# Performance work log

Measured on AMD Instinct MI355X. Metric: run time of the kernel, lower is better.

Reference implementation:

```python
import jax, jax.numpy as jnp
import numpy as np

IN_F, OUT_F, BLOCK, NBLK = 1024, 4096, 256, 16
TOPK = NBLK // 4  # 4, as in forward: n_blocks // 4


def setup_inputs() -> dict:
    key = jax.random.key(0)
    ks = jax.random.split(key, 7)
    s = 1.0 / np.sqrt(IN_F)
    s2 = 1.0 / np.sqrt(OUT_F)
    return {
        "x": jax.random.normal(ks[0], (4, 4096, IN_F), jnp.float32),
        "router_w": jax.random.uniform(ks[1], (NBLK, IN_F), jnp.float32, -s, s),
        "router_b": jax.random.uniform(ks[2], (NBLK,), jnp.float32, -s, s),
        "w1": jax.random.uniform(ks[3], (OUT_F, IN_F), jnp.float32, -s, s),
        "b1": jax.random.uniform(ks[4], (OUT_F,), jnp.float32, -s, s),
        "w2": jax.random.uniform(ks[5], (IN_F, OUT_F), jnp.float32, -s2, s2),
        "b2": jax.random.uniform(ks[6], (IN_F,), jnp.float32, -s2, s2),
    }


def reference(x, router_w, router_b, w1, b1, w2, b2):
    x_shape = x.shape
    xf = x.reshape(-1, IN_F)  # [N, d]
    n = xf.shape[0]
    # router: Linear + softmax, then top-k block selection per token
    prob = jax.nn.softmax(xf @ router_w.T + router_b, axis=-1)  # [N, n_blocks]
    _, idx = jax.lax.top_k(prob, TOPK)  # [N, k]
    mask = jnp.zeros((n, NBLK), bool).at[jnp.arange(n)[:, None], idx].set(True)
    # RoutedLinearRow: per-block fc1, zeros at unselected blocks
    w1b = w1.reshape(NBLK, BLOCK, IN_F)
    b1b = b1.reshape(NBLK, BLOCK)
    h = jnp.einsum('nd,ibd->nib', xf, w1b) + b1b  # [N, n_blocks, block]
    h = jnp.where(mask[:, :, None], h, jnp.zeros((), h.dtype))
    h = jax.nn.relu(h)
    # RoutedLinearCol: only selected blocks contribute
    w2b = w2.reshape(IN_F, NBLK, BLOCK)
    y = jnp.einsum('nib,dib->nd', jnp.where(mask[:, :, None], h, 0.0), w2b) + b2
    return y.reshape(x_shape)
```

## Files before the change

kernel.cpp:

```cpp
#include <hip/hip_runtime.h>
#include <hip/hip_bf16.h>

#define NTOK   16384
#define INF    1024
#define OUTF   4096
#define NBLK   16
#define BLKSZ  256
#define KTOP   4

typedef short bf16x8 __attribute__((ext_vector_type(8)));
typedef float f32x4 __attribute__((ext_vector_type(4)));
typedef unsigned short u16x8 __attribute__((ext_vector_type(8)));

__device__ __forceinline__ unsigned short f2bf(float f) {
  unsigned u = __float_as_uint(f);
  u += 0x7FFFu + ((u >> 16) & 1u);
  return (unsigned short)(u >> 16);
}

__device__ __forceinline__ void load_lds16(const void* g, void* l) {
  __builtin_amdgcn_global_load_lds(
      (const __attribute__((address_space(1))) unsigned int*)g,
      (__attribute__((address_space(3))) unsigned int*)l, 16, 0, 0);
}

__device__ __forceinline__ double shfl_xor_d(double v, int m) {
  long long l = __double_as_longlong(v);
  int lo = (int)(l & 0xFFFFFFFFll), hi = (int)(l >> 32);
  lo = __shfl_xor(lo, m);
  hi = __shfl_xor(hi, m);
  return __longlong_as_double(((long long)hi << 32) | (unsigned long long)(unsigned)lo);
}

__device__ __forceinline__ int pi_perm(int j) {
  return (j & 128) | ((j & 7) << 4) | ((j >> 3) & 15);
}

__global__ __launch_bounds__(256) void k_convert(
    const float* __restrict__ w1, const float* __restrict__ w2,
    const float* __restrict__ b1, unsigned short* __restrict__ w1b,
    unsigned short* __restrict__ w2p, float* __restrict__ b1p,
    unsigned* __restrict__ counts) {
  if (blockIdx.x == 0 && threadIdx.x < 16) counts[threadIdx.x] = 0;
  const size_t stride = (size_t)gridDim.x * 256;
  for (size_t i = (size_t)blockIdx.x * 256 + threadIdx.x; i < 1573376; i += stride) {
    if (i < 1048576) {
      float4 v = ((const float4*)w1)[i];
      ushort4 o;
      o.x = f2bf(v.x); o.y = f2bf(v.y); o.z = f2bf(v.z); o.w = f2bf(v.w);
      ((ushort4*)w1b)[i] = o;
    } else if (i < 1572864) {
      const size_t g = i - 1048576;
      const int d = (int)(g >> 9);
      const int rest = (int)(g & 511);
      const int jg = rest * 8;
      const int blk = jg >> 8;
      const int j0 = jg & 255;
      const float* src = w2 + (size_t)d * 4096 + blk * 256;
      u16x8 o;
#pragma unroll
      for (int ni = 0; ni < 8; ++ni) o[ni] = f2bf(src[pi_perm(j0 + ni)]);
      *(u16x8*)(w2p + (size_t)d * 4096 + jg) = o;
    } else {
      const int idx = (int)(i - 1572864);
      const int jg = idx * 8;
      const int blk = jg >> 8;
      const int j0 = jg & 255;
      const float* src = b1 + blk * 256;
      float o[8];
#pragma unroll
      for (int ni = 0; ni < 8; ++ni) o[ni] = src[pi_perm(j0 + ni)];
      float4* dst = (float4*)(b1p + jg);
      dst[0] = make_float4(o[0], o[1], o[2], o[3]);
      dst[1] = make_float4(o[4], o[5], o[6], o[7]);
    }
  }
}

__global__ __launch_bounds__(256) void k_router(
    const float* __restrict__ x, const float* __restrict__ rw,
    const float* __restrict__ rb, unsigned* __restrict__ tok_blocks,
    unsigned* __restrict__ counts, unsigned short* __restrict__ xb) {
  __shared__ float4 rwl[4096];
  const int tid = threadIdx.x;
  const float4* rw4 = (const float4*)rw;
  for (int i = tid; i < 4096; i += 256) rwl[i] = rw4[i];
  __syncthreads();

  const int n = blockIdx.x * 32 + (tid >> 3);
  const int q = tid & 7;
  double p[16];
#pragma unroll
  for (int j = 0; j < 16; ++j) p[j] = 0.0;
  const float4* xr = (const float4*)(x + (size_t)n * INF);
  ushort4* xbr = (ushort4*)(xb + (size_t)n * INF);
#pragma unroll 4
  for (int i = 0; i < 32; ++i) {
    const int d4 = q + i * 8;
    const float4 xv = xr[d4];
    ushort4 o;
    o.x = f2bf(xv.x); o.y = f2bf(xv.y); o.z = f2bf(xv.z); o.w = f2bf(xv.w);
    xbr[d4] = o;
#pragma unroll
    for (int j = 0; j < 16; ++j) {
      const float4 wv = rwl[j * 256 + d4];
      p[j] = fma((double)xv.x, (double)wv.x, p[j]);
      p[j] = fma((double)xv.y, (double)wv.y, p[j]);
      p[j] = fma((double)xv.z, (double)wv.z, p[j]);
      p[j] = fma((double)xv.w, (double)wv.w, p[j]);
    }
  }
#pragma unroll
  for (int j = 0; j < 16; ++j) {
    double v = p[j];
    v += shfl_xor_d(v, 1);
    v += shfl_xor_d(v, 2);
    v += shfl_xor_d(v, 4);
    p[j] = v + (double)rb[j];
  }

  __syncthreads();
  unsigned* hist = (unsigned*)rwl;
  if (tid < 16) hist[tid] = 0;
  __syncthreads();

  if (q == 0) {
    unsigned packed = 0;
#pragma unroll
    for (int j = 0; j < 16; ++j) {
      int r = 0;
#pragma unroll
      for (int j2 = 0; j2 < 16; ++j2)
        r += (int)((p[j2] > p[j]) | ((p[j2] == p[j]) & (j2 < j)));
      if (r < KTOP) packed |= (unsigned)j << (8 * r);
    }
    tok_blocks[n] = packed;
    atomicAdd(&hist[packed & 15u], 1u);
    atomicAdd(&hist[(packed >> 8) & 15u], 1u);
    atomicAdd(&hist[(packed >> 16) & 15u], 1u);
    atomicAdd(&hist[(packed >> 24) & 15u], 1u);
  }
  __syncthreads();
  if (tid < 16 && hist[tid]) atomicAdd(&counts[tid], hist[tid]);
}

__global__ void k_scan(const unsigned* __restrict__ counts, unsigned* __restrict__ off,
                       unsigned* __restrict__ cursors) {
  if (threadIdx.x == 0 && blockIdx.x == 0) {
    unsigned o = 0;
    for (int i = 0; i < 16; ++i) {
      off[i] = o; cursors[i] = o;
      o += (counts[i] + 127u) & ~127u;
    }
    off[16] = o;
  }
}

__global__ __launch_bounds__(256) void k_build(
    const unsigned* __restrict__ tok_blocks, unsigned* __restrict__ cursors,
    unsigned short* __restrict__ list) {
  const int n = blockIdx.x * 256 + threadIdx.x;
  const unsigned packed = tok_blocks[n];
  const int lane = threadIdx.x & 63;
  for (int b = 0; b < 16; ++b) {
    int r = -1;
#pragma unroll
    for (int q = 0; q < 4; ++q)
      if (((packed >> (8 * q)) & 15u) == (unsigned)b) r = q;
    unsigned long long m = __ballot(r >= 0);
    if (m) {
      int leader = __ffsll((unsigned long long)m) - 1;
      unsigned base = 0;
      if (lane == leader) base = atomicAdd(&cursors[b], (unsigned)__popcll(m));
      base = (unsigned)__shfl((int)base, leader);
      if (r >= 0) {
        unsigned pos = base + (unsigned)__popcll(m & ((1ull << lane) - 1ull));
        list[pos] = (unsigned short)(n | (r << 14));
      }
    }
  }
}

__global__ __launch_bounds__(512, 1) void k_ffn(
    const unsigned short* __restrict__ xb, const unsigned short* __restrict__ w1b,
    const unsigned short* __restrict__ w2p, const float* __restrict__ b1p,
    const unsigned short* __restrict__ list, const unsigned* __restrict__ counts,
    const unsigned* __restrict__ off, unsigned short* __restrict__ part) {
  __shared__ __align__(16) char lds[163840];
  char* const As0 = lds + 65536;
  char* const As1 = lds + 81920;
  char* const Bs0 = lds + 98304;
  char* const Bs1 = lds + 131072;

  const int bid0 = blockIdx.x;
  const int bid = (bid0 & 7) * 256 + (bid0 >> 3);
  const int blk = bid >> 7;
  const int tile = bid & 127;
  const unsigned cnt = counts[blk];
  if ((unsigned)(tile * 128) >= cnt) return;
  const unsigned goff = off[blk] + tile * 128;
  const int rem = (int)cnt - tile * 128;

  const int tid = threadIdx.x;
  const int lane = tid & 63;
  const int wid = tid >> 6;
  const int wr = wid >> 1;
  const int wc = wid & 1;
  const int asl = tid & 7;
  const int c16 = lane & 15;

  const unsigned tok0 = list[goff + (tid >> 3)] & 0x3FFFu;
  const unsigned tok1 = list[goff + 64 + (tid >> 3)] & 0x3FFFu;
  const int arow0 = tid >> 3;
  const int arow1 = 64 + arow0;

  unsigned ep[2][4];
#pragma unroll
  for (int mi = 0; mi < 2; ++mi)
#pragma unroll
    for (int i = 0; i < 4; ++i)
      ep[mi][i] = list[goff + wr * 32 + mi * 16 + (lane >> 4) * 4 + i];

#define STAGE_A(buf, k0)                                                        \
  {                                                                             \
    load_lds16(xb + (size_t)tok0 * INF + (k0) + (asl ^ (arow0 & 7)) * 8,        \
               (buf) + (wid * 64) * 16);                                        \
    load_lds16(xb + (size_t)tok1 * INF + (k0) + (asl ^ (arow1 & 7)) * 8,        \
               (buf) + (512 + wid * 64) * 16);                                  \
  }

#define STAGE_B1(buf, k0)                                                       \
  _Pragma("unroll")                                                             \
  for (int r = 0; r < 4; ++r) {                                                 \
    const int row = (r * 512 + tid) >> 3;                                       \
    load_lds16(w1b + ((size_t)(blk * 256 + row)) * INF + (k0) +                 \
                   (asl ^ (row & 7)) * 8,                                       \
               (buf) + (r * 512 + wid * 64) * 16);                              \
  }

#define COMPUTE_A(abuf, bbuf)                                                   \
  _Pragma("unroll")                                                             \
  for (int ks = 0; ks < 2; ++ks) {                                              \
    const int kc = ks * 4 + (lane >> 4);                                        \
    bf16x8 a[2], b[8];                                                          \
    _Pragma("unroll")                                                           \
    for (int mi = 0; mi < 2; ++mi) {                                            \
      const int row = wr * 32 + mi * 16 + (lane & 15);                          \
      a[mi] = *(const bf16x8*)((abuf) + row * 128 + ((kc ^ (row & 7)) << 4));   \
    }                                                                           \
    _Pragma("unroll")                                                           \
    for (int ni = 0; ni < 8; ++ni) {                                            \
      const int row = wc * 128 + ni * 16 + (lane & 15);                         \
      b[ni] = *(const bf16x8*)((bbuf) + row * 128 + ((kc ^ (row & 7)) << 4));   \
    }                                                                           \
    _Pragma("unroll")                                                           \
    for (int mi = 0; mi < 2; ++mi)                                              \
      _Pragma("unroll")                                                         \
      for (int ni = 0; ni < 8; ++ni)                                            \
        acc[mi][ni] =                                                           \
            __builtin_amdgcn_mfma_f32_16x16x32_bf16(a[mi], b[ni], acc[mi][ni], 0, 0, 0); \
  }

  f32x4 acc[2][8] = {};
  STAGE_A(As0, 0);
  STAGE_B1(Bs0, 0);
  __syncthreads();
#pragma unroll 1
  for (int kk = 0; kk < 8; ++kk) {
    const int k0 = kk * 128;
    STAGE_A(As1, k0 + 64);
    STAGE_B1(Bs1, k0 + 64);
    COMPUTE_A(As0, Bs0);
    __syncthreads();
    if (kk < 7) {
      STAGE_A(As0, k0 + 128);
      STAGE_B1(Bs0, k0 + 128);
    }
    COMPUTE_A(As1, Bs1);
    __syncthreads();
  }

#define STAGE_B2(buf, it)                                                       \
  {                                                                             \
    const int ns2 = (it) >> 2, k02 = ((it) & 3) * 64;                           \
    _Pragma("unroll")                                                           \
    for (int r = 0; r < 4; ++r) {                                               \
      const int row = (r * 512 + tid) >> 3;                                     \
      load_lds16(w2p + (size_t)(ns2 * 256 + row) * OUTF + blk * 256 + k02 +     \
                     (asl ^ (row & 7)) * 8,                                     \
                 (buf) + (r * 512 + wid * 64) * 16);                            \
    }                                                                           \
  }

#define COMPUTE_B(bbuf, k02)                                                    \
  _Pragma("unroll")                                                             \
  for (int ks = 0; ks < 2; ++ks) {                                              \
    const int kc = ks * 4 + (lane >> 4);                                        \
    bf16x8 a[2], b[8];                                                          \
    _Pragma("unroll")                                                           \
    for (int mi = 0; mi < 2; ++mi) {                                            \
      const int row = wr * 32 + mi * 16 + (lane & 15);                          \
      a[mi] = *(const bf16x8*)(lds + row * 512 + (k02) * 2 +                    \
                               ((kc ^ (row & 7)) << 4));                        \
    }                                                                           \
    _Pragma("unroll")                                                           \
    for (int ni = 0; ni < 8; ++ni) {                                            \
      const int row = wc * 128 + ni * 16 + (lane & 15);                         \
      b[ni] = *(const bf16x8*)((bbuf) + row * 128 + ((kc ^ (row & 7)) << 4));   \
    }                                                                           \
    _Pragma("unroll")                                                           \
    for (int mi = 0; mi < 2; ++mi)                                              \
      _Pragma("unroll")                                                         \
      for (int ni = 0; ni < 8; ++ni)                                            \
        acc2[mi][ni] =                                                          \
            __builtin_amdgcn_mfma_f32_16x16x32_bf16(a[mi], b[ni], acc2[mi][ni], 0, 0, 0); \
  }

  STAGE_B2(Bs0, 0);

  {
    const float4* bp = (const float4*)(b1p + blk * 256 + wc * 128 + c16 * 8);
    const float4 bv0 = bp[0], bv1 = bp[1];
    const float bvv[8] = {bv0.x, bv0.y, bv0.z, bv0.w, bv1.x, bv1.y, bv1.z, bv1.w};
    const int chunk = wc * 16 + c16;
    const int cslot = (chunk & ~7);
    const int clow  = (chunk & 7);
#pragma unroll
    for (int mi = 0; mi < 2; ++mi) {
#pragma unroll
      for (int i = 0; i < 4; ++i) {
        const int row = wr * 32 + mi * 16 + (lane >> 4) * 4 + i;
        u16x8 wv;
#pragma unroll
        for (int ni = 0; ni < 8; ++ni) {
          float v = acc[mi][ni][i] + bvv[ni];
          v = v > 0.f ? v : 0.f;
          wv[ni] = f2bf(v);
        }
        *(u16x8*)(lds + row * 512 + ((cslot | (clow ^ (row & 7))) << 4)) = wv;
      }
    }
  }
  __syncthreads();

#pragma unroll 1
  for (int ns = 0; ns < 4; ++ns) {
    f32x4 acc2[2][8] = {};
    const int it0 = ns * 4;
    STAGE_B2(Bs1, it0 + 1);
    COMPUTE_B(Bs0, 0);
    __syncthreads();
    STAGE_B2(Bs0, it0 + 2);
    COMPUTE_B(Bs1, 64);
    __syncthreads();
    STAGE_B2(Bs1, it0 + 3);
    COMPUTE_B(Bs0, 128);
    __syncthreads();
    if (ns < 3) STAGE_B2(Bs0, it0 + 4);
    COMPUTE_B(Bs1, 192);
    __syncthreads();
#pragma unroll
    for (int mi = 0; mi < 2; ++mi) {
#pragma unroll
      for (int i = 0; i < 4; ++i) {
        const int row = wr * 32 + mi * 16 + (lane >> 4) * 4 + i;
        if (row < rem) {
          const unsigned e = ep[mi][i];
          u16x8 wv;
#pragma unroll
          for (int ni = 0; ni < 8; ++ni) wv[ni] = f2bf(acc2[mi][ni][i]);
          *(u16x8*)(part + ((size_t)(e & 0x3FFFu) * 4 + (e >> 14)) * 1024 +
                    ns * 256 + wc * 128 + c16 * 8) = wv;
        }
      }
    }
  }
#undef STAGE_A
#undef STAGE_B1
#undef STAGE_B2
#undef COMPUTE_A
#undef COMPUTE_B
}

__global__ __launch_bounds__(256) void k_reduce(const unsigned short* __restrict__ part,
                                                const float* __restrict__ b2,
                                                float* __restrict__ out) {
  __shared__ float lds[8 * 1028];
  const int tid = threadIdx.x;
  const int tok0 = blockIdx.x * 8;
  const int tok_l = tid >> 5;
  const int l32 = tid & 31;
  const unsigned short* pbase = part + (size_t)(tok0 + tok_l) * 4096;

#pragma unroll
  for (int g = 0; g < 4; ++g) {
    const int idx = g * 32 + l32;
    const int p0 = idx * 8;
    float s[8] = {0.f, 0.f, 0.f, 0.f, 0.f, 0.f, 0.f, 0.f};
#pragma unroll
    for (int sl = 0; sl < 4; ++sl) {
      u16x8 v = *(const u16x8*)(pbase + sl * 1024 + p0);
#pragma unroll
      for (int j = 0; j < 8; ++j)
        s[j] += __uint_as_float((unsigned)(unsigned short)v[j] << 16);
    }
    const int ns = idx >> 5, wcb = (idx >> 4) & 1, cc = idx & 15;
#pragma unroll
    for (int ni = 0; ni < 8; ++ni)
      lds[tok_l * 1028 + ns * 256 + wcb * 128 + ni * 16 + cc] = s[ni];
  }
  __syncthreads();
  const float4 b2v = ((const float4*)b2)[tid];
#pragma unroll
  for (int r = 0; r < 8; ++r) {
    f32x4 lv = *(f32x4*)&lds[r * 1028 + tid * 4];
    float4 o = make_float4(lv[0] + b2v.x, lv[1] + b2v.y, lv[2] + b2v.z, lv[3] + b2v.w);
    *(float4*)(out + (size_t)(tok0 + r) * 1024 + tid * 4) = o;
  }
}

extern "C" void kernel_launch(void* const* d_in, const int* in_sizes, int n_in,
                              void* d_out, int out_size, void* d_ws, size_t ws_size,
                              hipStream_t stream) {
  const float* x  = (const float*)d_in[0];
  const float* rw = (const float*)d_in[1];
  const float* rb = (const float*)d_in[2];
  const float* w1 = (const float*)d_in[3];
  const float* b1 = (const float*)d_in[4];
  const float* w2 = (const float*)d_in[5];
  const float* b2 = (const float*)d_in[6];
  float* out = (float*)d_out;

  char* ws = (char*)d_ws;
  unsigned short* part = (unsigned short*)(ws);
  unsigned short* xb   = (unsigned short*)(ws + 134217728);
  unsigned short* w1b  = (unsigned short*)(ws + 167772160);
  unsigned short* w2p  = (unsigned short*)(ws + 176160768);
  unsigned* tokb       = (unsigned*)(ws + 184549376);
  unsigned short* list = (unsigned short*)(ws + 184614912);
  float* b1p           = (float*)(ws + 184750080);
  unsigned* counts     = (unsigned*)(ws + 184766464);
  unsigned* off        = (unsigned*)(ws + 184766528);
  unsigned* cursors    = (unsigned*)(ws + 184766656);

  k_convert<<<dim3(1024), dim3(256), 0, stream>>>(w1, w2, b1, w1b, w2p, b1p, counts);
  k_router<<<dim3(512), dim3(256), 0, stream>>>(x, rw, rb, tokb, counts, xb);
  k_scan<<<dim3(1), dim3(64), 0, stream>>>(counts, off, cursors);
  k_build<<<dim3(64), dim3(256), 0, stream>>>(tokb, cursors, list);
  k_ffn<<<dim3(2048), dim3(512), 0, stream>>>(xb, w1b, w2p, b1p, list, counts, off, part);
  k_reduce<<<dim3(2048), dim3(256), 0, stream>>>(part, b2, out);
}
```

Measured before the change: 260.2 us.

## Fuse weight conversion into router, drop scan kernel, halve FFN block threads

Merges the weight-conversion kernel into the router kernel and removes the scan kernel. k_build and k_ffn now recompute the block offsets from counts, and counts/alloc are zeroed with a memset. The FFN kernel goes from 512 to 256 threads per block, so each wave handles 64 rows (4 MFMA row tiles) instead of 32. This doubles per-wave accumulator registers and A-fragment reuse. The goal is fewer launches and less LDS traffic per MFMA, at the risk of register pressure and lower wave count per CU.

```diff
diff --git a/kernel.cpp b/kernel.cpp
--- a/kernel.cpp
+++ b/kernel.cpp
@@ -36,14 +36,77 @@
   return (j & 128) | ((j & 7) << 4) | ((j >> 3) & 15);
 }
 
-__global__ __launch_bounds__(256) void k_convert(
-    const float* __restrict__ w1, const float* __restrict__ w2,
-    const float* __restrict__ b1, unsigned short* __restrict__ w1b,
-    unsigned short* __restrict__ w2p, float* __restrict__ b1p,
-    unsigned* __restrict__ counts) {
-  if (blockIdx.x == 0 && threadIdx.x < 16) counts[threadIdx.x] = 0;
+__global__ __launch_bounds__(256) void k_cvt_router(
+    const float* __restrict__ x, const float* __restrict__ rw,
+    const float* __restrict__ rb, const float* __restrict__ w1,
+    const float* __restrict__ w2, const float* __restrict__ b1,
+    unsigned* __restrict__ tok_blocks, unsigned* __restrict__ counts,
+    unsigned short* __restrict__ xb, unsigned short* __restrict__ w1b,
+    unsigned short* __restrict__ w2p, float* __restrict__ b1p) {
+  __shared__ float4 rwl[4096];
+  const int tid = threadIdx.x;
+  const float4* rw4 = (const float4*)rw;
+  for (int i = tid; i < 4096; i += 256) rwl[i] = rw4[i];
+  __syncthreads();
+
+  const int n = blockIdx.x * 32 + (tid >> 3);
+  const int q = tid & 7;
+  double p[16];
+#pragma unroll
+  for (int j = 0; j < 16; ++j) p[j] = 0.0;
+  const float4* xr = (const float4*)(x + (size_t)n * INF);
+  ushort4* xbr = (ushort4*)(xb + (size_t)n * INF);
+#pragma unroll 4
+  for (int i = 0; i < 32; ++i) {
+    const int d4 = q + i * 8;
+    const float4 xv = xr[d4];
+    ushort4 o;
+    o.x = f2bf(xv.x); o.y = f2bf(xv.y); o.z = f2bf(xv.z); o.w = f2bf(xv.w);
+    xbr[d4] = o;
+#pragma unroll
+    for (int j = 0; j < 16; ++j) {
+      const float4 wv = rwl[j * 256 + d4];
+      p[j] = fma((double)xv.x, (double)wv.x, p[j]);
+      p[j] = fma((double)xv.y, (double)wv.y, p[j]);
+      p[j] = fma((double)xv.z, (double)wv.z, p[j]);
+      p[j] = fma((double)xv.w, (double)wv.w, p[j]);
+    }
+  }
+#pragma unroll
+  for (int j = 0; j < 16; ++j) {
+    double v = p[j];
+    v += shfl_xor_d(v, 1);
+    v += shfl_xor_d(v, 2);
+    v += shfl_xor_d(v, 4);
+    p[j] = v + (double)rb[j];
+  }
+
+  __syncthreads();
+  unsigned* hist = (unsigned*)rwl;
+  if (tid < 16) hist[tid] = 0;
+  __syncthreads();
+
+  if (q == 0) {
+    unsigned packed = 0;
+#pragma unroll
+    for (int j = 0; j < 16; ++j) {
+      int r = 0;
+#pragma unroll
+      for (int j2 = 0; j2 < 16; ++j2)
+        r += (int)((p[j2] > p[j]) | ((p[j2] == p[j]) & (j2 < j)));
+      if (r < KTOP) packed |= (unsigned)j << (8 * r);
+    }
+    tok_blocks[n] = packed;
+    atomicAdd(&hist[packed & 15u], 1u);
+    atomicAdd(&hist[(packed >> 8) & 15u], 1u);
+    atomicAdd(&hist[(packed >> 16) & 15u], 1u);
+    atomicAdd(&hist[(packed >> 24) & 15u], 1u);
+  }
+  __syncthreads();
+  if (tid < 16 && hist[tid]) atomicAdd(&counts[tid], hist[tid]);
+
   const size_t stride = (size_t)gridDim.x * 256;
-  for (size_t i = (size_t)blockIdx.x * 256 + threadIdx.x; i < 1573376; i += stride) {
+  for (size_t i = (size_t)blockIdx.x * 256 + tid; i < 1573376; i += stride) {
     if (i < 1048576) {
       float4 v = ((const float4*)w1)[i];
       ushort4 o;
@@ -77,91 +140,19 @@
   }
 }
 
-__global__ __launch_bounds__(256) void k_router(
-    const float* __restrict__ x, const float* __restrict__ rw,
-    const float* __restrict__ rb, unsigned* __restrict__ tok_blocks,
-    unsigned* __restrict__ counts, unsigned short* __restrict__ xb) {
-  __shared__ float4 rwl[4096];
-  const int tid = threadIdx.x;
-  const float4* rw4 = (const float4*)rw;
-  for (int i = tid; i < 4096; i += 256) rwl[i] = rw4[i];
-  __syncthreads();
-
-  const int n = blockIdx.x * 32 + (tid >> 3);
-  const int q = tid & 7;
-  double p[16];
-#pragma unroll
-  for (int j = 0; j < 16; ++j) p[j] = 0.0;
-  const float4* xr = (const float4*)(x + (size_t)n * INF);
-  ushort4* xbr = (ushort4*)(xb + (size_t)n * INF);
-#pragma unroll 4
-  for (int i = 0; i < 32; ++i) {
-    const int d4 = q + i * 8;
-    const float4 xv = xr[d4];
-    ushort4 o;
-    o.x = f2bf(xv.x); o.y = f2bf(xv.y); o.z = f2bf(xv.z); o.w = f2bf(xv.w);
-    xbr[d4] = o;
-#pragma unroll
-    for (int j = 0; j < 16; ++j) {
-      const float4 wv = rwl[j * 256 + d4];
-      p[j] = fma((double)xv.x, (double)wv.x, p[j]);
-      p[j] = fma((double)xv.y, (double)wv.y, p[j]);
-      p[j] = fma((double)xv.z, (double)wv.z, p[j]);
-      p[j] = fma((double)xv.w, (double)wv.w, p[j]);
-    }
-  }
-#pragma unroll
-  for (int j = 0; j < 16; ++j) {
-    double v = p[j];
-    v += shfl_xor_d(v, 1);
-    v += shfl_xor_d(v, 2);
-    v += shfl_xor_d(v, 4);
-    p[j] = v + (double)rb[j];
-  }
-
-  __syncthreads();
-  unsigned* hist = (unsigned*)rwl;
-  if (tid < 16) hist[tid] = 0;
-  __syncthreads();
-
-  if (q == 0) {
-    unsigned packed = 0;
-#pragma unroll
-    for (int j = 0; j < 16; ++j) {
-      int r = 0;
-#pragma unroll
-      for (int j2 = 0; j2 < 16; ++j2)
-        r += (int)((p[j2] > p[j]) | ((p[j2] == p[j]) & (j2 < j)));
-      if (r < KTOP) packed |= (unsigned)j << (8 * r);
-    }
-    tok_blocks[n] = packed;
-    atomicAdd(&hist[packed & 15u], 1u);
-    atomicAdd(&hist[(packed >> 8) & 15u], 1u);
-    atomicAdd(&hist[(packed >> 16) & 15u], 1u);
-    atomicAdd(&hist[(packed >> 24) & 15u], 1u);
-  }
-  __syncthreads();
-  if (tid < 16 && hist[tid]) atomicAdd(&counts[tid], hist[tid]);
-}
-
-__global__ void k_scan(const unsigned* __restrict__ counts, unsigned* __restrict__ off,
-                       unsigned* __restrict__ cursors) {
-  if (threadIdx.x == 0 && blockIdx.x == 0) {
+__global__ __launch_bounds__(256) void k_build(
+    const unsigned* __restrict__ tok_blocks, const unsigned* __restrict__ counts,
+    unsigned* __restrict__ alloc, unsigned short* __restrict__ list) {
+  unsigned offl[16];
+  {
     unsigned o = 0;
-    for (int i = 0; i < 16; ++i) {
-      off[i] = o; cursors[i] = o;
-      o += (counts[i] + 127u) & ~127u;
-    }
-    off[16] = o;
-  }
-}
-
-__global__ __launch_bounds__(256) void k_build(
-    const unsigned* __restrict__ tok_blocks, unsigned* __restrict__ cursors,
-    unsigned short* __restrict__ list) {
+#pragma unroll
+    for (int i = 0; i < 16; ++i) { offl[i] = o; o += (counts[i] + 127u) & ~127u; }
+  }
   const int n = blockIdx.x * 256 + threadIdx.x;
   const unsigned packed = tok_blocks[n];
   const int lane = threadIdx.x & 63;
+#pragma unroll
   for (int b = 0; b < 16; ++b) {
     int r = -1;
 #pragma unroll
@@ -171,7 +162,7 @@
     if (m) {
       int leader = __ffsll((unsigned long long)m) - 1;
       unsigned base = 0;
-      if (lane == leader) base = atomicAdd(&cursors[b], (unsigned)__popcll(m));
+      if (lane == leader) base = offl[b] + atomicAdd(&alloc[b], (unsigned)__popcll(m));
       base = (unsigned)__shfl((int)base, leader);
       if (r >= 0) {
         unsigned pos = base + (unsigned)__popcll(m & ((1ull << lane) - 1ull));
@@ -181,11 +172,11 @@
   }
 }
 
-__global__ __launch_bounds__(512, 1) void k_ffn(
+__global__ __launch_bounds__(256, 1) void k_ffn(
     const unsigned short* __restrict__ xb, const unsigned short* __restrict__ w1b,
     const unsigned short* __restrict__ w2p, const float* __restrict__ b1p,
     const unsigned short* __restrict__ list, const unsigned* __restrict__ counts,
-    const unsigned* __restrict__ off, unsigned short* __restrict__ part) {
+    unsigned short* __restrict__ part) {
   __shared__ __align__(16) char lds[163840];
   char* const As0 = lds + 65536;
   char* const As1 = lds + 81920;
@@ -196,9 +187,18 @@
   const int bid = (bid0 & 7) * 256 + (bid0 >> 3);
   const int blk = bid >> 7;
   const int tile = bid & 127;
-  const unsigned cnt = counts[blk];
+  unsigned cnt = 0, goffBase = 0;
+  {
+    unsigned o = 0;
+#pragma unroll
+    for (int i = 0; i < 16; ++i) {
+      const unsigned c = counts[i];
+      if (i == blk) { cnt = c; goffBase = o; }
+      o += (c + 127u) & ~127u;
+    }
+  }
   if ((unsigned)(tile * 128) >= cnt) return;
-  const unsigned goff = off[blk] + tile * 128;
+  const unsigned goff = goffBase + tile * 128;
   const int rem = (int)cnt - tile * 128;
 
   const int tid = threadIdx.x;
@@ -206,62 +206,50 @@
   const int wid = tid >> 6;
   const int wr = wid >> 1;
   const int wc = wid & 1;
-  const int asl = tid & 7;
   const int c16 = lane & 15;
-
-  const unsigned tok0 = list[goff + (tid >> 3)] & 0x3FFFu;
-  const unsigned tok1 = list[goff + 64 + (tid >> 3)] & 0x3FFFu;
-  const int arow0 = tid >> 3;
-  const int arow1 = 64 + arow0;
-
-  unsigned ep[2][4];
-#pragma unroll
-  for (int mi = 0; mi < 2; ++mi)
-#pragma unroll
-    for (int i = 0; i < 4; ++i)
-      ep[mi][i] = list[goff + wr * 32 + mi * 16 + (lane >> 4) * 4 + i];
+  const int aChunk = (tid & 7) ^ ((tid >> 3) & 7);
+
+  unsigned tok[4];
+#pragma unroll
+  for (int l = 0; l < 4; ++l) tok[l] = list[goff + (tid >> 3) + l * 32] & 0x3FFFu;
 
 #define STAGE_A(buf, k0)                                                        \
-  {                                                                             \
-    load_lds16(xb + (size_t)tok0 * INF + (k0) + (asl ^ (arow0 & 7)) * 8,        \
-               (buf) + (wid * 64) * 16);                                        \
-    load_lds16(xb + (size_t)tok1 * INF + (k0) + (asl ^ (arow1 & 7)) * 8,        \
-               (buf) + (512 + wid * 64) * 16);                                  \
-  }
+  _Pragma("unroll")                                                             \
+  for (int l = 0; l < 4; ++l)                                                   \
+    load_lds16(xb + (size_t)tok[l] * 1024 + (k0) + aChunk * 8,                  \
+               (buf) + (l * 256 + wid * 64) * 16);
 
 #define STAGE_B1(buf, k0)                                                       \
   _Pragma("unroll")                                                             \
-  for (int r = 0; r < 4; ++r) {                                                 \
-    const int row = (r * 512 + tid) >> 3;                                       \
-    load_lds16(w1b + ((size_t)(blk * 256 + row)) * INF + (k0) +                 \
-                   (asl ^ (row & 7)) * 8,                                       \
-               (buf) + (r * 512 + wid * 64) * 16);                              \
-  }
+  for (int l = 0; l < 8; ++l)                                                   \
+    load_lds16(w1b + (size_t)(blk * 256 + l * 32 + (tid >> 3)) * 1024 + (k0) +  \
+                   aChunk * 8,                                                  \
+               (buf) + (l * 256 + wid * 64) * 16);
 
 #define COMPUTE_A(abuf, bbuf)                                                   \
   _Pragma("unroll")                                                             \
   for (int ks = 0; ks < 2; ++ks) {                                              \
     const int kc = ks * 4 + (lane >> 4);                                        \
-    bf16x8 a[2], b[8];                                                          \
-    _Pragma("unroll")                                                           \
-    for (int mi = 0; mi < 2; ++mi) {                                            \
-      const int row = wr * 32 + mi * 16 + (lane & 15);                          \
+    bf16x8 a[4], b[8];                                                          \
+    _Pragma("unroll")                                                           \
+    for (int mi = 0; mi < 4; ++mi) {                                            \
+      const int row = wr * 64 + mi * 16 + c16;                                  \
       a[mi] = *(const bf16x8*)((abuf) + row * 128 + ((kc ^ (row & 7)) << 4));   \
     }                                                                           \
     _Pragma("unroll")                                                           \
     for (int ni = 0; ni < 8; ++ni) {                                            \
-      const int row = wc * 128 + ni * 16 + (lane & 15);                         \
+      const int row = wc * 128 + ni * 16 + c16;                                 \
       b[ni] = *(const bf16x8*)((bbuf) + row * 128 + ((kc ^ (row & 7)) << 4));   \
     }                                                                           \
     _Pragma("unroll")                                                           \
-    for (int mi = 0; mi < 2; ++mi)                                              \
+    for (int mi = 0; mi < 4; ++mi)                                              \
       _Pragma("unroll")                                                         \
       for (int ni = 0; ni < 8; ++ni)                                            \
         acc[mi][ni] =                                                           \
             __builtin_amdgcn_mfma_f32_16x16x32_bf16(a[mi], b[ni], acc[mi][ni], 0, 0, 0); \
   }
 
-  f32x4 acc[2][8] = {};
+  f32x4 acc[4][8] = {};
   STAGE_A(As0, 0);
   STAGE_B1(Bs0, 0);
   __syncthreads();
@@ -284,32 +272,30 @@
   {                                                                             \
     const int ns2 = (it) >> 2, k02 = ((it) & 3) * 64;                           \
     _Pragma("unroll")                                                           \
-    for (int r = 0; r < 4; ++r) {                                               \
-      const int row = (r * 512 + tid) >> 3;                                     \
-      load_lds16(w2p + (size_t)(ns2 * 256 + row) * OUTF + blk * 256 + k02 +     \
-                     (asl ^ (row & 7)) * 8,                                     \
-                 (buf) + (r * 512 + wid * 64) * 16);                            \
-    }                                                                           \
+    for (int l = 0; l < 8; ++l)                                                 \
+      load_lds16(w2p + (size_t)(ns2 * 256 + l * 32 + (tid >> 3)) * 4096 +       \
+                     blk * 256 + k02 + aChunk * 8,                              \
+                 (buf) + (l * 256 + wid * 64) * 16);                            \
   }
 
 #define COMPUTE_B(bbuf, k02)                                                    \
   _Pragma("unroll")                                                             \
   for (int ks = 0; ks < 2; ++ks) {                                              \
     const int kc = ks * 4 + (lane >> 4);                                        \
-    bf16x8 a[2], b[8];                                                          \
-    _Pragma("unroll")                                                           \
-    for (int mi = 0; mi < 2; ++mi) {                                            \
-      const int row = wr * 32 + mi * 16 + (lane & 15);                          \
+    bf16x8 a[4], b[8];                                                          \
+    _Pragma("unroll")                                                           \
+    for (int mi = 0; mi < 4; ++mi) {                                            \
+      const int row = wr * 64 + mi * 16 + c16;                                  \
       a[mi] = *(const bf16x8*)(lds + row * 512 + (k02) * 2 +                    \
                                ((kc ^ (row & 7)) << 4));                        \
     }                                                                           \
     _Pragma("unroll")                                                           \
     for (int ni = 0; ni < 8; ++ni) {                                            \
-      const int row = wc * 128 + ni * 16 + (lane & 15);                         \
+      const int row = wc * 128 + ni * 16 + c16;                                 \
       b[ni] = *(const bf16x8*)((bbuf) + row * 128 + ((kc ^ (row & 7)) << 4));   \
     }                                                                           \
     _Pragma("unroll")                                                           \
-    for (int mi = 0; mi < 2; ++mi)                                              \
+    for (int mi = 0; mi < 4; ++mi)                                              \
       _Pragma("unroll")                                                         \
       for (int ni = 0; ni < 8; ++ni)                                            \
         acc2[mi][ni] =                                                          \
@@ -326,10 +312,10 @@
     const int cslot = (chunk & ~7);
     const int clow  = (chunk & 7);
 #pragma unroll
-    for (int mi = 0; mi < 2; ++mi) {
+    for (int mi = 0; mi < 4; ++mi) {
 #pragma unroll
       for (int i = 0; i < 4; ++i) {
-        const int row = wr * 32 + mi * 16 + (lane >> 4) * 4 + i;
+        const int row = wr * 64 + mi * 16 + (lane >> 4) * 4 + i;
         u16x8 wv;
 #pragma unroll
         for (int ni = 0; ni < 8; ++ni) {
@@ -345,7 +331,7 @@
 
 #pragma unroll 1
   for (int ns = 0; ns < 4; ++ns) {
-    f32x4 acc2[2][8] = {};
+    f32x4 acc2[4][8] = {};
     const int it0 = ns * 4;
     STAGE_B2(Bs1, it0 + 1);
     COMPUTE_B(Bs0, 0);
@@ -360,12 +346,12 @@
     COMPUTE_B(Bs1, 192);
     __syncthreads();
 #pragma unroll
-    for (int mi = 0; mi < 2; ++mi) {
+    for (int mi = 0; mi < 4; ++mi) {
 #pragma unroll
       for (int i = 0; i < 4; ++i) {
-        const int row = wr * 32 + mi * 16 + (lane >> 4) * 4 + i;
+        const int row = wr * 64 + mi * 16 + (lane >> 4) * 4 + i;
         if (row < rem) {
-          const unsigned e = ep[mi][i];
+          const unsigned e = list[goff + row];
           u16x8 wv;
 #pragma unroll
           for (int ni = 0; ni < 8; ++ni) wv[ni] = f2bf(acc2[mi][ni][i]);
@@ -440,13 +426,12 @@
   unsigned short* list = (unsigned short*)(ws + 184614912);
   float* b1p           = (float*)(ws + 184750080);
   unsigned* counts     = (unsigned*)(ws + 184766464);
-  unsigned* off        = (unsigned*)(ws + 184766528);
-  unsigned* cursors    = (unsigned*)(ws + 184766656);
-
-  k_convert<<<dim3(1024), dim3(256), 0, stream>>>(w1, w2, b1, w1b, w2p, b1p, counts);
-  k_router<<<dim3(512), dim3(256), 0, stream>>>(x, rw, rb, tokb, counts, xb);
-  k_scan<<<dim3(1), dim3(64), 0, stream>>>(counts, off, cursors);
-  k_build<<<dim3(64), dim3(256), 0, stream>>>(tokb, cursors, list);
-  k_ffn<<<dim3(2048), dim3(512), 0, stream>>>(xb, w1b, w2p, b1p, list, counts, off, part);
+  unsigned* alloc      = (unsigned*)(ws + 184766528);
+
+  hipMemsetAsync(ws + 184766464, 0, 128, stream);
+  k_cvt_router<<<dim3(512), dim3(256), 0, stream>>>(x, rw, rb, w1, w2, b1, tokb,
+                                                    counts, xb, w1b, w2p, b1p);
+  k_build<<<dim3(64), dim3(256), 0, stream>>>(tokb, counts, alloc, list);
+  k_ffn<<<dim3(2048), dim3(256), 0, stream>>>(xb, w1b, w2p, b1p, list, counts, part);
   k_reduce<<<dim3(2048), dim3(256), 0, stream>>>(part, b2, out);
 }
```

After: 290.6 us. 1.12x slower.

## Fuse weight conversion into router, drop scan kernel, preload fc2 A fragments

Applied to the files above, without the earlier changes.

Merges the weight-conversion kernel into the router kernel and removes the single-thread scan kernel, so each consumer recomputes block offsets from counts and a memset zeroes the counters. This cuts two launches and their serialization gaps. In the FFN kernel, the relu'd hidden-tile A fragments are loaded from LDS into registers once instead of on every second-GEMM substep. The register-resident fragments add register pressure, and the fused kernel now runs conversion on 512 blocks instead of 1024.

```diff
diff --git a/kernel.cpp b/kernel.cpp
--- a/kernel.cpp
+++ b/kernel.cpp
@@ -36,14 +36,77 @@
   return (j & 128) | ((j & 7) << 4) | ((j >> 3) & 15);
 }
 
-__global__ __launch_bounds__(256) void k_convert(
-    const float* __restrict__ w1, const float* __restrict__ w2,
-    const float* __restrict__ b1, unsigned short* __restrict__ w1b,
-    unsigned short* __restrict__ w2p, float* __restrict__ b1p,
-    unsigned* __restrict__ counts) {
-  if (blockIdx.x == 0 && threadIdx.x < 16) counts[threadIdx.x] = 0;
+__global__ __launch_bounds__(256) void k_cvt_router(
+    const float* __restrict__ x, const float* __restrict__ rw,
+    const float* __restrict__ rb, const float* __restrict__ w1,
+    const float* __restrict__ w2, const float* __restrict__ b1,
+    unsigned* __restrict__ tok_blocks, unsigned* __restrict__ counts,
+    unsigned short* __restrict__ xb, unsigned short* __restrict__ w1b,
+    unsigned short* __restrict__ w2p, float* __restrict__ b1p) {
+  __shared__ float4 rwl[4096];
+  const int tid = threadIdx.x;
+  const float4* rw4 = (const float4*)rw;
+  for (int i = tid; i < 4096; i += 256) rwl[i] = rw4[i];
+  __syncthreads();
+
+  const int n = blockIdx.x * 32 + (tid >> 3);
+  const int q = tid & 7;
+  double p[16];
+#pragma unroll
+  for (int j = 0; j < 16; ++j) p[j] = 0.0;
+  const float4* xr = (const float4*)(x + (size_t)n * INF);
+  ushort4* xbr = (ushort4*)(xb + (size_t)n * INF);
+#pragma unroll 4
+  for (int i = 0; i < 32; ++i) {
+    const int d4 = q + i * 8;
+    const float4 xv = xr[d4];
+    ushort4 o;
+    o.x = f2bf(xv.x); o.y = f2bf(xv.y); o.z = f2bf(xv.z); o.w = f2bf(xv.w);
+    xbr[d4] = o;
+#pragma unroll
+    for (int j = 0; j < 16; ++j) {
+      const float4 wv = rwl[j * 256 + d4];
+      p[j] = fma((double)xv.x, (double)wv.x, p[j]);
+      p[j] = fma((double)xv.y, (double)wv.y, p[j]);
+      p[j] = fma((double)xv.z, (double)wv.z, p[j]);
+      p[j] = fma((double)xv.w, (double)wv.w, p[j]);
+    }
+  }
+#pragma unroll
+  for (int j = 0; j < 16; ++j) {
+    double v = p[j];
+    v += shfl_xor_d(v, 1);
+    v += shfl_xor_d(v, 2);
+    v += shfl_xor_d(v, 4);
+    p[j] = v + (double)rb[j];
+  }
+
+  __syncthreads();
+  unsigned* hist = (unsigned*)rwl;
+  if (tid < 16) hist[tid] = 0;
+  __syncthreads();
+
+  if (q == 0) {
+    unsigned packed = 0;
+#pragma unroll
+    for (int j = 0; j < 16; ++j) {
+      int r = 0;
+#pragma unroll
+      for (int j2 = 0; j2 < 16; ++j2)
+        r += (int)((p[j2] > p[j]) | ((p[j2] == p[j]) & (j2 < j)));
+      if (r < KTOP) packed |= (unsigned)j << (8 * r);
+    }
+    tok_blocks[n] = packed;
+    atomicAdd(&hist[packed & 15u], 1u);
+    atomicAdd(&hist[(packed >> 8) & 15u], 1u);
+    atomicAdd(&hist[(packed >> 16) & 15u], 1u);
+    atomicAdd(&hist[(packed >> 24) & 15u], 1u);
+  }
+  __syncthreads();
+  if (tid < 16 && hist[tid]) atomicAdd(&counts[tid], hist[tid]);
+
   const size_t stride = (size_t)gridDim.x * 256;
-  for (size_t i = (size_t)blockIdx.x * 256 + threadIdx.x; i < 1573376; i += stride) {
+  for (size_t i = (size_t)blockIdx.x * 256 + tid; i < 1573376; i += stride) {
     if (i < 1048576) {
       float4 v = ((const float4*)w1)[i];
       ushort4 o;
@@ -77,91 +140,19 @@
   }
 }
 
-__global__ __launch_bounds__(256) void k_router(
-    const float* __restrict__ x, const float* __restrict__ rw,
-    const float* __restrict__ rb, unsigned* __restrict__ tok_blocks,
-    unsigned* __restrict__ counts, unsigned short* __restrict__ xb) {
-  __shared__ float4 rwl[4096];
-  const int tid = threadIdx.x;
-  const float4* rw4 = (const float4*)rw;
-  for (int i = tid; i < 4096; i += 256) rwl[i] = rw4[i];
-  __syncthreads();
-
-  const int n = blockIdx.x * 32 + (tid >> 3);
-  const int q = tid & 7;
-  double p[16];
-#pragma unroll
-  for (int j = 0; j < 16; ++j) p[j] = 0.0;
-  const float4* xr = (const float4*)(x + (size_t)n * INF);
-  ushort4* xbr = (ushort4*)(xb + (size_t)n * INF);
-#pragma unroll 4
-  for (int i = 0; i < 32; ++i) {
-    const int d4 = q + i * 8;
-    const float4 xv = xr[d4];
-    ushort4 o;
-    o.x = f2bf(xv.x); o.y = f2bf(xv.y); o.z = f2bf(xv.z); o.w = f2bf(xv.w);
-    xbr[d4] = o;
-#pragma unroll
-    for (int j = 0; j < 16; ++j) {
-      const float4 wv = rwl[j * 256 + d4];
-      p[j] = fma((double)xv.x, (double)wv.x, p[j]);
-      p[j] = fma((double)xv.y, (double)wv.y, p[j]);
-      p[j] = fma((double)xv.z, (double)wv.z, p[j]);
-      p[j] = fma((double)xv.w, (double)wv.w, p[j]);
-    }
-  }
-#pragma unroll
-  for (int j = 0; j < 16; ++j) {
-    double v = p[j];
-    v += shfl_xor_d(v, 1);
-    v += shfl_xor_d(v, 2);
-    v += shfl_xor_d(v, 4);
-    p[j] = v + (double)rb[j];
-  }
-
-  __syncthreads();
-  unsigned* hist = (unsigned*)rwl;
-  if (tid < 16) hist[tid] = 0;
-  __syncthreads();
-
-  if (q == 0) {
-    unsigned packed = 0;
-#pragma unroll
-    for (int j = 0; j < 16; ++j) {
-      int r = 0;
-#pragma unroll
-      for (int j2 = 0; j2 < 16; ++j2)
-        r += (int)((p[j2] > p[j]) | ((p[j2] == p[j]) & (j2 < j)));
-      if (r < KTOP) packed |= (unsigned)j << (8 * r);
-    }
-    tok_blocks[n] = packed;
-    atomicAdd(&hist[packed & 15u], 1u);
-    atomicAdd(&hist[(packed >> 8) & 15u], 1u);
-    atomicAdd(&hist[(packed >> 16) & 15u], 1u);
-    atomicAdd(&hist[(packed >> 24) & 15u], 1u);
-  }
-  __syncthreads();
-  if (tid < 16 && hist[tid]) atomicAdd(&counts[tid], hist[tid]);
-}
-
-__global__ void k_scan(const unsigned* __restrict__ counts, unsigned* __restrict__ off,
-                       unsigned* __restrict__ cursors) {
-  if (threadIdx.x == 0 && blockIdx.x == 0) {
+__global__ __launch_bounds__(256) void k_build(
+    const unsigned* __restrict__ tok_blocks, const unsigned* __restrict__ counts,
+    unsigned* __restrict__ alloc, unsigned short* __restrict__ list) {
+  unsigned offl[16];
+  {
     unsigned o = 0;
-    for (int i = 0; i < 16; ++i) {
-      off[i] = o; cursors[i] = o;
-      o += (counts[i] + 127u) & ~127u;
-    }
-    off[16] = o;
-  }
-}
-
-__global__ __launch_bounds__(256) void k_build(
-    const unsigned* __restrict__ tok_blocks, unsigned* __restrict__ cursors,
-    unsigned short* __restrict__ list) {
+#pragma unroll
+    for (int i = 0; i < 16; ++i) { offl[i] = o; o += (counts[i] + 127u) & ~127u; }
+  }
   const int n = blockIdx.x * 256 + threadIdx.x;
   const unsigned packed = tok_blocks[n];
   const int lane = threadIdx.x & 63;
+#pragma unroll
   for (int b = 0; b < 16; ++b) {
     int r = -1;
 #pragma unroll
@@ -171,7 +162,7 @@
     if (m) {
       int leader = __ffsll((unsigned long long)m) - 1;
       unsigned base = 0;
-      if (lane == leader) base = atomicAdd(&cursors[b], (unsigned)__popcll(m));
+      if (lane == leader) base = offl[b] + atomicAdd(&alloc[b], (unsigned)__popcll(m));
       base = (unsigned)__shfl((int)base, leader);
       if (r >= 0) {
         unsigned pos = base + (unsigned)__popcll(m & ((1ull << lane) - 1ull));
@@ -185,7 +176,7 @@
     const unsigned short* __restrict__ xb, const unsigned short* __restrict__ w1b,
     const unsigned short* __restrict__ w2p, const float* __restrict__ b1p,
     const unsigned short* __restrict__ list, const unsigned* __restrict__ counts,
-    const unsigned* __restrict__ off, unsigned short* __restrict__ part) {
+    unsigned short* __restrict__ part) {
   __shared__ __align__(16) char lds[163840];
   char* const As0 = lds + 65536;
   char* const As1 = lds + 81920;
@@ -196,9 +187,18 @@
   const int bid = (bid0 & 7) * 256 + (bid0 >> 3);
   const int blk = bid >> 7;
   const int tile = bid & 127;
-  const unsigned cnt = counts[blk];
+  unsigned cnt = 0, goffBase = 0;
+  {
+    unsigned o = 0;
+#pragma unroll
+    for (int i = 0; i < 16; ++i) {
+      const unsigned c = counts[i];
+      if (i == blk) { cnt = c; goffBase = o; }
+      o += (c + 127u) & ~127u;
+    }
+  }
   if ((unsigned)(tile * 128) >= cnt) return;
-  const unsigned goff = off[blk] + tile * 128;
+  const unsigned goff = goffBase + tile * 128;
   const int rem = (int)cnt - tile * 128;
 
   const int tid = threadIdx.x;
@@ -245,12 +245,12 @@
     bf16x8 a[2], b[8];                                                          \
     _Pragma("unroll")                                                           \
     for (int mi = 0; mi < 2; ++mi) {                                            \
-      const int row = wr * 32 + mi * 16 + (lane & 15);                          \
+      const int row = wr * 32 + mi * 16 + c16;                                  \
       a[mi] = *(const bf16x8*)((abuf) + row * 128 + ((kc ^ (row & 7)) << 4));   \
     }                                                                           \
     _Pragma("unroll")                                                           \
     for (int ni = 0; ni < 8; ++ni) {                                            \
-      const int row = wc * 128 + ni * 16 + (lane & 15);                         \
+      const int row = wc * 128 + ni * 16 + c16;                                 \
       b[ni] = *(const bf16x8*)((bbuf) + row * 128 + ((kc ^ (row & 7)) << 4));   \
     }                                                                           \
     _Pragma("unroll")                                                           \
@@ -292,28 +292,22 @@
     }                                                                           \
   }
 
-#define COMPUTE_B(bbuf, k02)                                                    \
+#define COMPUTE_B(bbuf, kg)                                                     \
   _Pragma("unroll")                                                             \
   for (int ks = 0; ks < 2; ++ks) {                                              \
     const int kc = ks * 4 + (lane >> 4);                                        \
-    bf16x8 a[2], b[8];                                                          \
-    _Pragma("unroll")                                                           \
-    for (int mi = 0; mi < 2; ++mi) {                                            \
-      const int row = wr * 32 + mi * 16 + (lane & 15);                          \
-      a[mi] = *(const bf16x8*)(lds + row * 512 + (k02) * 2 +                    \
-                               ((kc ^ (row & 7)) << 4));                        \
-    }                                                                           \
+    bf16x8 b[8];                                                                \
     _Pragma("unroll")                                                           \
     for (int ni = 0; ni < 8; ++ni) {                                            \
-      const int row = wc * 128 + ni * 16 + (lane & 15);                         \
+      const int row = wc * 128 + ni * 16 + c16;                                 \
       b[ni] = *(const bf16x8*)((bbuf) + row * 128 + ((kc ^ (row & 7)) << 4));   \
     }                                                                           \
     _Pragma("unroll")                                                           \
     for (int mi = 0; mi < 2; ++mi)                                              \
       _Pragma("unroll")                                                         \
       for (int ni = 0; ni < 8; ++ni)                                            \
-        acc2[mi][ni] =                                                          \
-            __builtin_amdgcn_mfma_f32_16x16x32_bf16(a[mi], b[ni], acc2[mi][ni], 0, 0, 0); \
+        acc2[mi][ni] = __builtin_amdgcn_mfma_f32_16x16x32_bf16(                 \
+            pa[mi][ks][kg], b[ni], acc2[mi][ni], 0, 0, 0);                      \
   }
 
   STAGE_B2(Bs0, 0);
@@ -343,6 +337,20 @@
   }
   __syncthreads();
 
+  bf16x8 pa[2][2][4];
+#pragma unroll
+  for (int mi = 0; mi < 2; ++mi) {
+    const int row = wr * 32 + mi * 16 + c16;
+#pragma unroll
+    for (int ks = 0; ks < 2; ++ks) {
+      const int kc = ks * 4 + (lane >> 4);
+#pragma unroll
+      for (int kg = 0; kg < 4; ++kg)
+        pa[mi][ks][kg] = *(const bf16x8*)(lds + row * 512 + kg * 128 +
+                                          ((kc ^ (row & 7)) << 4));
+    }
+  }
+
 #pragma unroll 1
   for (int ns = 0; ns < 4; ++ns) {
     f32x4 acc2[2][8] = {};
@@ -351,13 +359,13 @@
     COMPUTE_B(Bs0, 0);
     __syncthreads();
     STAGE_B2(Bs0, it0 + 2);
-    COMPUTE_B(Bs1, 64);
+    COMPUTE_B(Bs1, 1);
     __syncthreads();
     STAGE_B2(Bs1, it0 + 3);
-    COMPUTE_B(Bs0, 128);
+    COMPUTE_B(Bs0, 2);
     __syncthreads();
     if (ns < 3) STAGE_B2(Bs0, it0 + 4);
-    COMPUTE_B(Bs1, 192);
+    COMPUTE_B(Bs1, 3);
     __syncthreads();
 #pragma unroll
     for (int mi = 0; mi < 2; ++mi) {
@@ -440,13 +448,12 @@
   unsigned short* list = (unsigned short*)(ws + 184614912);
   float* b1p           = (float*)(ws + 184750080);
   unsigned* counts     = (unsigned*)(ws + 184766464);
-  unsigned* off        = (unsigned*)(ws + 184766528);
-  unsigned* cursors    = (unsigned*)(ws + 184766656);
-
-  k_convert<<<dim3(1024), dim3(256), 0, stream>>>(w1, w2, b1, w1b, w2p, b1p, counts);
-  k_router<<<dim3(512), dim3(256), 0, stream>>>(x, rw, rb, tokb, counts, xb);
-  k_scan<<<dim3(1), dim3(64), 0, stream>>>(counts, off, cursors);
-  k_build<<<dim3(64), dim3(256), 0, stream>>>(tokb, cursors, list);
-  k_ffn<<<dim3(2048), dim3(512), 0, stream>>>(xb, w1b, w2p, b1p, list, counts, off, part);
+  unsigned* alloc      = (unsigned*)(ws + 184766528);
+
+  hipMemsetAsync(ws + 184766464, 0, 128, stream);
+  k_cvt_router<<<dim3(512), dim3(256), 0, stream>>>(x, rw, rb, w1, w2, b1, tokb,
+                                                    counts, xb, w1b, w2p, b1p);
+  k_build<<<dim3(64), dim3(256), 0, stream>>>(tokb, counts, alloc, list);
+  k_ffn<<<dim3(2048), dim3(512), 0, stream>>>(xb, w1b, w2p, b1p, list, counts, part);
   k_reduce<<<dim3(2048), dim3(256), 0, stream>>>(part, b2, out);
 }
```

Result: no change. 259.5 us, median of 4 (-0.3%).
